# Optimization experiments

Hardware: AMD Instinct MI355X
Metric: run time of the kernel (lower is better)

## Reference

```python
import jax, jax.numpy as jnp
import numpy as np

D_MODEL = 512
NUM_HEADS = 8
VOCAB = 32000
B, TQ, TS = 4, 512, 512


def setup_inputs() -> dict:
    key = jax.random.key(0)
    ks = jax.random.split(key, 12)
    s = 1.0 / np.sqrt(D_MODEL)
    inp = {
        "src_vocab_size": VOCAB,
        "dec_output": jax.random.normal(ks[0], (B, TQ, D_MODEL), jnp.float32),
        "enc_output": jax.random.normal(ks[1], (B, TS, D_MODEL), jnp.float32),
        "src": jax.random.randint(ks[2], (B, TS), 0, VOCAB),
        "p1": jax.random.uniform(ks[3], (B, TQ, VOCAB), jnp.float32),
        # fcQ: d_model -> d_model (xavier)
        "WfcQ": jax.random.normal(ks[4], (D_MODEL, D_MODEL), jnp.float32) * s,
        "bfcQ": jnp.zeros((D_MODEL,), jnp.float32),
        # MHA query / key projections (V and output proj skipped in copy mode)
        "Wq": jax.random.normal(ks[5], (D_MODEL, D_MODEL), jnp.float32) * s,
        "bq": jnp.zeros((D_MODEL,), jnp.float32),
        "Wk": jax.random.normal(ks[6], (D_MODEL, D_MODEL), jnp.float32) * s,
        "bk": jnp.zeros((D_MODEL,), jnp.float32),
        # fcw: d_model -> 1 gate
        "Wfcw": jax.random.normal(ks[7], (1, D_MODEL), jnp.float32) * s,
        "bfcw": jnp.zeros((1,), jnp.float32),
    }
    return inp


def reference(src_vocab_size, dec_output, enc_output, src, p1,
              WfcQ, bfcQ, Wq, bq, Wk, bk, Wfcw, bfcw):
    b, tq, d = dec_output.shape
    h = NUM_HEADS
    dh = d // h
    # copy_query = fcQ(dec_output)
    cq = dec_output @ WfcQ.T + bfcQ
    # per-head Q, K projections
    Q = (cq @ Wq.T + bq).reshape(b, tq, h, dh).transpose(0, 2, 1, 3)          # [b,h,tq,dh]
    K = (enc_output @ Wk.T + bk).reshape(b, -1, h, dh).transpose(0, 2, 1, 3)  # [b,h,ts,dh]
    scale = 1.0 / jnp.sqrt(jnp.asarray(dh, dec_output.dtype))
    scores = jnp.einsum('bhqd,bhkd->bhqk', Q, K) * scale
    attn = jax.nn.softmax(scores, axis=-1).mean(axis=1)  # [b,tq,ts] head-averaged
    # attn @ one_hot(src, vocab)  ==  scatter-add of attn weights by src token id
    def scatter_copy(a, s):  # a: [tq,ts], s: [ts]
        return jax.ops.segment_sum(a.T, s, num_segments=src_vocab_size).T  # [tq,vocab]
    a_output = jax.vmap(scatter_copy)(attn, src)  # [b,tq,vocab]
    p2 = jax.nn.softmax(a_output, axis=-1)
    w = jax.nn.sigmoid(dec_output @ Wfcw.T + bfcw)  # [b,tq,1]
    return p2 * w + (1.0 - w) * p1
```

## Files before the change

kernel.cpp:

```cpp
#include <hip/hip_runtime.h>

constexpr int BATCH = 4;
constexpr int SEQ   = 512;
constexpr int DM    = 512;
constexpr int NH    = 8;
constexpr int NV    = 32000;
constexpr int NROWS = BATCH * SEQ;

typedef short short8 __attribute__((ext_vector_type(8)));
typedef float floatx4 __attribute__((ext_vector_type(4)));
typedef float floatv4 __attribute__((ext_vector_type(4)));

__device__ __forceinline__ float wave_reduce_max(float v) {
#pragma unroll
  for (int o = 32; o > 0; o >>= 1) v = fmaxf(v, __shfl_down(v, o, 64));
  return v;
}
__device__ __forceinline__ float wave_reduce_sum(float v) {
#pragma unroll
  for (int o = 32; o > 0; o >>= 1) v += __shfl_down(v, o, 64);
  return v;
}
__device__ __forceinline__ unsigned short f2bf(float f) {
  unsigned u = __float_as_uint(f);
  u += 0x7FFFu + ((u >> 16) & 1u);
  return (unsigned short)(u >> 16);
}
__device__ __forceinline__ float bf2f(unsigned short b) {
  return __uint_as_float(((unsigned)b) << 16);
}

__global__ __launch_bounds__(256)
void prep_kernel(const float* __restrict__ dec, const float* __restrict__ enc,
                 const float* __restrict__ Wk,
                 unsigned short* __restrict__ dec_bf, unsigned short* __restrict__ enc_bf,
                 unsigned short* __restrict__ wk_bf,
                 const int* __restrict__ src, int* __restrict__ map,
                 const float* __restrict__ Wq, const float* __restrict__ WfcQ,
                 unsigned short* __restrict__ wqc_bf,
                 const float* __restrict__ bfcQ, const float* __restrict__ bq,
                 float* __restrict__ bq2) {
  __shared__ float As[16][68];
  __shared__ float Bs[16][68];
  const int b = blockIdx.x, tid = threadIdx.x;
  if (b < 64) {
    const int m0 = (b >> 3) << 6, n0 = (b & 7) << 6;
    const int tx = tid & 15, ty = tid >> 4;
    const int r = tid >> 2, c = (tid & 3) << 2;
    float acc[4][4] = {};
    for (int k0 = 0; k0 < DM; k0 += 16) {
      const float4 av = *(const float4*)(Wq + (size_t)(m0 + r) * DM + k0 + c);
      As[c + 0][r] = av.x; As[c + 1][r] = av.y; As[c + 2][r] = av.z; As[c + 3][r] = av.w;
      const float4 bv = *(const float4*)(WfcQ + (size_t)(k0 + ty) * DM + n0 + (tx << 2));
      *(float4*)(&Bs[ty][tx << 2]) = bv;
      __syncthreads();
#pragma unroll
      for (int kk = 0; kk < 16; ++kk) {
        const float4 a4 = *(const float4*)(&As[kk][ty << 2]);
        const float4 b4 = *(const float4*)(&Bs[kk][tx << 2]);
        const float a[4] = {a4.x, a4.y, a4.z, a4.w};
        const float bb[4] = {b4.x, b4.y, b4.z, b4.w};
#pragma unroll
        for (int i = 0; i < 4; ++i)
#pragma unroll
          for (int j = 0; j < 4; ++j) acc[i][j] = fmaf(a[i], bb[j], acc[i][j]);
      }
      __syncthreads();
    }
#pragma unroll
    for (int i = 0; i < 4; ++i)
#pragma unroll
      for (int j = 0; j < 4; ++j)
        wqc_bf[(size_t)(m0 + (ty << 2) + i) * DM + n0 + (tx << 2) + j] = f2bf(acc[i][j]);
  } else if (b < 2368) {
    const int cb = b - 64;
    const float* in; unsigned short* outp; int i;
    if (cb < 1024)      { in = dec; outp = dec_bf; i = cb * 256 + tid; }
    else if (cb < 2048) { in = enc; outp = enc_bf; i = (cb - 1024) * 256 + tid; }
    else                { in = Wk;  outp = wk_bf;  i = (cb - 2048) * 256 + tid; }
    const float4 v = ((const float4*)in)[i];
    ushort4 o;
    o.x = f2bf(v.x); o.y = f2bf(v.y); o.z = f2bf(v.z); o.w = f2bf(v.w);
    ((ushort4*)outp)[i] = o;
  } else if (b < 2372) {
    const int bb = b - 2368;
    const int v0 = src[bb * SEQ + tid];
    atomicCAS(&map[(size_t)bb * NV + v0], -1, tid);
    const int v1 = src[bb * SEQ + tid + 256];
    atomicCAS(&map[(size_t)bb * NV + v1], -1, tid + 256);
  } else {
    const int h = tid >> 6, l = tid & 63;
    const int n = (b - 2372) * 4 + h;
    float s = 0.f;
#pragma unroll
    for (int t = 0; t < 8; ++t) {
      const int j = l + 64 * t;
      s = fmaf(Wq[(size_t)n * DM + j], bfcQ[j], s);
    }
    s = wave_reduce_sum(s);
    if (l == 0) bq2[n] = bq[n] + s;
  }
}

__global__ __launch_bounds__(256)
void gemm_mfma_kernel(const unsigned short* __restrict__ A0, const unsigned short* __restrict__ W0,
                      const float* __restrict__ b0, unsigned short* __restrict__ C0,
                      const unsigned short* __restrict__ A1, const unsigned short* __restrict__ W1,
                      const float* __restrict__ b1, unsigned short* __restrict__ C1) {
  const unsigned short* A; const unsigned short* W; const float* bias; unsigned short* C;
  if (blockIdx.z == 0) { A = A0; W = W0; bias = b0; C = C0; }
  else                 { A = A1; W = W1; bias = b1; C = C1; }
  const int m0 = blockIdx.y << 6, n0 = blockIdx.x << 6;
  __shared__ __align__(16) unsigned short As[64 * 72];
  __shared__ __align__(16) unsigned short Ws[64 * 72];
  const int tid = threadIdx.x;
  const int wv = tid >> 6, l = tid & 63;
  const int lm = l & 15, lq = l >> 4;
  floatx4 acc[4] = {};
  for (int k0 = 0; k0 < DM; k0 += 64) {
#pragma unroll
    for (int i = 0; i < 2; ++i) {
      const int ch = tid + (i << 8);
      const int row = ch >> 3, c8 = (ch & 7) << 3;
      *(int4*)(&As[row * 72 + c8]) = *(const int4*)(A + (size_t)(m0 + row) * DM + k0 + c8);
      *(int4*)(&Ws[row * 72 + c8]) = *(const int4*)(W + (size_t)(n0 + row) * DM + k0 + c8);
    }
    __syncthreads();
#pragma unroll
    for (int ks = 0; ks < 64; ks += 32) {
      const short8 a = *(const short8*)(&As[(16 * wv + lm) * 72 + ks + lq * 8]);
#pragma unroll
      for (int c = 0; c < 4; ++c) {
        const short8 b = *(const short8*)(&Ws[(16 * c + lm) * 72 + ks + lq * 8]);
        acc[c] = __builtin_amdgcn_mfma_f32_16x16x32_bf16(a, b, acc[c], 0, 0, 0);
      }
    }
    __syncthreads();
  }
#pragma unroll
  for (int c = 0; c < 4; ++c) {
    const float bv = bias[n0 + 16 * c + lm];
#pragma unroll
    for (int r = 0; r < 4; ++r)
      As[(16 * wv + lq * 4 + r) * 72 + 16 * c + lm] = f2bf(acc[c][r] + bv);
  }
  __syncthreads();
#pragma unroll
  for (int i = 0; i < 2; ++i) {
    const int idx = tid + (i << 8);
    const int row = idx >> 3, c8 = (idx & 7) << 3;
    *(int4*)(C + (size_t)(m0 + row) * DM + n0 + c8) = *(const int4*)(&As[row * 72 + c8]);
  }
}

__global__ __launch_bounds__(256)
void scores_mfma_kernel(const unsigned short* __restrict__ Q, const unsigned short* __restrict__ Kk,
                        unsigned short* __restrict__ scores) {
  const int bh = blockIdx.z, bb = bh >> 3, h = bh & 7;
  const int tq0 = blockIdx.y << 6, ts0 = blockIdx.x << 6;
  __shared__ __align__(16) unsigned short Qs[64 * 72];
  __shared__ __align__(16) unsigned short Ks[64 * 72];
  const int tid = threadIdx.x;
  const int wv = tid >> 6, l = tid & 63;
  const int lm = l & 15, lq = l >> 4;
#pragma unroll
  for (int i = 0; i < 2; ++i) {
    const int ch = tid + (i << 8);
    const int row = ch >> 3, c8 = (ch & 7) << 3;
    *(int4*)(&Qs[row * 72 + c8]) =
        *(const int4*)(Q + (size_t)(bb * SEQ + tq0 + row) * DM + h * 64 + c8);
    *(int4*)(&Ks[row * 72 + c8]) =
        *(const int4*)(Kk + (size_t)(bb * SEQ + ts0 + row) * DM + h * 64 + c8);
  }
  __syncthreads();
  floatx4 acc[4] = {};
#pragma unroll
  for (int ks = 0; ks < 64; ks += 32) {
    const short8 a = *(const short8*)(&Qs[(16 * wv + lm) * 72 + ks + lq * 8]);
#pragma unroll
    for (int c = 0; c < 4; ++c) {
      const short8 b = *(const short8*)(&Ks[(16 * c + lm) * 72 + ks + lq * 8]);
      acc[c] = __builtin_amdgcn_mfma_f32_16x16x32_bf16(a, b, acc[c], 0, 0, 0);
    }
  }
  __syncthreads();
#pragma unroll
  for (int c = 0; c < 4; ++c)
#pragma unroll
    for (int r = 0; r < 4; ++r)
      Qs[(16 * wv + lq * 4 + r) * 72 + 16 * c + lm] = f2bf(acc[c][r] * 0.125f);
  __syncthreads();
#pragma unroll
  for (int i = 0; i < 2; ++i) {
    const int idx = tid + (i << 8);
    const int row = idx >> 3, c8 = (idx & 7) << 3;
    *(int4*)(scores + ((size_t)bh * SEQ + tq0 + row) * SEQ + ts0 + c8) =
        *(const int4*)(&Qs[row * 72 + c8]);
  }
}

__global__ __launch_bounds__(512)
void softmax_fused_kernel(const unsigned short* __restrict__ scores, const int* __restrict__ src,
                          const int* __restrict__ map, const float* __restrict__ dec,
                          const float* __restrict__ Wfcw, const float* __restrict__ bfcw,
                          float* __restrict__ expa, float* __restrict__ row_a,
                          float* __restrict__ row_b) {
  __shared__ float hp[8 * 520];
  __shared__ float aslot[512];
  __shared__ float r1[8], r2[8];
  const int row = blockIdx.x, bb = row >> 9, tq = row & 511;
  const int tid = threadIdx.x, h = tid >> 6, l = tid & 63;
  aslot[tid] = 0.f;
  const unsigned short* srow = scores + ((size_t)(bb * NH + h) * SEQ + tq) * SEQ;
  union { int4 v; unsigned short u[8]; } U;
  U.v = *(const int4*)(srow + 8 * l);
  float s[8];
#pragma unroll
  for (int i = 0; i < 8; ++i) s[i] = bf2f(U.u[i]);
  float m = s[0];
#pragma unroll
  for (int i = 1; i < 8; ++i) m = fmaxf(m, s[i]);
  m = wave_reduce_max(m);
  m = __shfl(m, 0, 64);
  float e[8], sum = 0.f;
#pragma unroll
  for (int i = 0; i < 8; ++i) { e[i] = __expf(s[i] - m); sum += e[i]; }
  sum = wave_reduce_sum(sum);
  sum = __shfl(sum, 0, 64);
  const float inv = 1.f / sum;
  float4 p0, p1v;
  p0.x = e[0] * inv; p0.y = e[1] * inv; p0.z = e[2] * inv; p0.w = e[3] * inv;
  p1v.x = e[4] * inv; p1v.y = e[5] * inv; p1v.z = e[6] * inv; p1v.w = e[7] * inv;
  *(float4*)(&hp[h * 520 + 8 * l])     = p0;
  *(float4*)(&hp[h * 520 + 8 * l + 4]) = p1v;
  __syncthreads();
  float a = 0.f;
#pragma unroll
  for (int h2 = 0; h2 < 8; ++h2) a += hp[h2 * 520 + tid];
  a *= 0.125f;
  const int sv = src[bb * SEQ + tid];
  const int rep = map[(size_t)bb * NV + sv];
  atomicAdd(&aslot[rep], a);
  __syncthreads();
  const float ev = __expf(aslot[tid]);
  expa[(size_t)row * SEQ + tid] = ev;
  const float d = dec[(size_t)row * DM + tid] * Wfcw[tid];
  float es = wave_reduce_sum(ev);
  float ds = wave_reduce_sum(d);
  if (l == 0) { r1[h] = es; r2[h] = ds; }
  __syncthreads();
  if (tid == 0) {
    float esum = 0.f, dsum = bfcw[0];
#pragma unroll
    for (int i = 0; i < 8; ++i) { esum += r1[i]; dsum += r2[i]; }
    const float w = 1.f / (1.f + __expf(-dsum));
    row_a[row] = 1.f - w;
    row_b[row] = w / ((float)(NV - SEQ) + esum);
  }
}

__global__ __launch_bounds__(320)
void final_kernel(const float* __restrict__ p1, const int* __restrict__ map,
                  const float* __restrict__ expa, const float* __restrict__ row_a,
                  const float* __restrict__ row_b, float* __restrict__ out) {
  const int row = blockIdx.y;
  const int q4  = blockIdx.x * 320 + threadIdx.x;
  const int bb  = row >> 9;
  const size_t g = (size_t)row * (NV / 4) + q4;
  const floatv4 p = __builtin_nontemporal_load((const floatv4*)p1 + g);
  const int4 m = *(const int4*)(map + (size_t)bb * NV + (q4 << 2));
  const float ra = row_a[row], rb = row_b[row];
  const float* ea = expa + (size_t)row * SEQ;
  const float t0 = ea[m.x & 511];
  const float t1 = ea[m.y & 511];
  const float t2 = ea[m.z & 511];
  const float t3 = ea[m.w & 511];
  const float e0 = (m.x >= 0) ? t0 : 1.f;
  const float e1 = (m.y >= 0) ? t1 : 1.f;
  const float e2 = (m.z >= 0) ? t2 : 1.f;
  const float e3 = (m.w >= 0) ? t3 : 1.f;
  floatv4 o;
  o.x = fmaf(ra, p.x, rb * e0);
  o.y = fmaf(ra, p.y, rb * e1);
  o.z = fmaf(ra, p.z, rb * e2);
  o.w = fmaf(ra, p.w, rb * e3);
  __builtin_nontemporal_store(o, (floatv4*)out + g);
}

extern "C" void kernel_launch(void* const* d_in, const int* in_sizes, int n_in,
                              void* d_out, int out_size, void* d_ws, size_t ws_size,
                              hipStream_t stream) {
  const float* dec  = (const float*)d_in[1];
  const float* enc  = (const float*)d_in[2];
  const int*   src  = (const int*)d_in[3];
  const float* p1   = (const float*)d_in[4];
  const float* WfcQ = (const float*)d_in[5];
  const float* bfcQ = (const float*)d_in[6];
  const float* Wq   = (const float*)d_in[7];
  const float* bq   = (const float*)d_in[8];
  const float* Wk   = (const float*)d_in[9];
  const float* bk   = (const float*)d_in[10];
  const float* Wfcw = (const float*)d_in[11];
  const float* bfcw = (const float*)d_in[12];
  float* out = (float*)d_out;

  char* ws = (char*)d_ws;
  int*            map     = (int*)(ws);
  unsigned short* dec_bf  = (unsigned short*)(ws + (size_t)( 1 << 20));
  unsigned short* enc_bf  = (unsigned short*)(ws + (size_t)( 3 << 20));
  unsigned short* wk_bf   = (unsigned short*)(ws + (size_t)( 5 << 20));
  unsigned short* wqc_bf  = (unsigned short*)(ws + (size_t)( 5 << 20) + (512 << 10));
  float*          bq2     = (float*)(ws + (size_t)( 6 << 20));
  float*          row_a   = (float*)(ws + (size_t)( 6 << 20) + (64 << 10));
  float*          row_b   = (float*)(ws + (size_t)( 6 << 20) + (128 << 10));
  unsigned short* qlin_bf = (unsigned short*)(ws + (size_t)( 7 << 20));
  unsigned short* klin_bf = (unsigned short*)(ws + (size_t)( 9 << 20));
  float*          expa    = (float*)(ws + (size_t)(11 << 20));
  unsigned short* scores  = (unsigned short*)(ws + (size_t)(16 << 20));

  hipMemsetAsync(map, 0xFF, (size_t)BATCH * NV * sizeof(int), stream);

  prep_kernel<<<2500, 256, 0, stream>>>(dec, enc, Wk, dec_bf, enc_bf, wk_bf,
                                        src, map, Wq, WfcQ, wqc_bf, bfcQ, bq, bq2);

  gemm_mfma_kernel<<<dim3(8, 32, 2), 256, 0, stream>>>(
      dec_bf, wqc_bf, bq2, qlin_bf, enc_bf, wk_bf, bk, klin_bf);

  scores_mfma_kernel<<<dim3(8, 8, 32), 256, 0, stream>>>(qlin_bf, klin_bf, scores);

  softmax_fused_kernel<<<NROWS, 512, 0, stream>>>(scores, src, map, dec, Wfcw, bfcw,
                                                  expa, row_a, row_b);

  final_kernel<<<dim3(25, NROWS), 320, 0, stream>>>(p1, map, expa, row_a, row_b, out);
}
```

Measured before the change: 510.2 us.

## Fuse attention scores and softmax into one kernel, fold map init into prep

The separate scores MFMA kernel and the per-row softmax kernel are replaced by a single attn_kernel. In it, each wave computes one head's QK^T for 8 query rows over all 512 keys in registers, then does the softmax, head averaging via LDS atomics, the scatter by source token, the exp, and the gate reduction. This removes the bf16 scores buffer round trip through global memory and one kernel launch. The hipMemsetAsync of the map is replaced by in-kernel initialization inside the map-building blocks of prep_kernel. The cost is a large register footprint (32 accumulator tiles), half-wasted MFMA rows (16-row tiles for 8 query rows), LDS atomics, and only 256 blocks to cover the GPU.

```diff
diff --git a/kernel.cpp b/kernel.cpp
--- a/kernel.cpp
+++ b/kernel.cpp
@@ -84,6 +84,10 @@
     ((ushort4*)outp)[i] = o;
   } else if (b < 2372) {
     const int bb = b - 2368;
+    int4* mp = (int4*)(map + (size_t)bb * NV);
+    const int4 neg = make_int4(-1, -1, -1, -1);
+    for (int i = tid; i < NV / 4; i += 256) mp[i] = neg;
+    __syncthreads();
     const int v0 = src[bb * SEQ + tid];
     atomicCAS(&map[(size_t)bb * NV + v0], -1, tid);
     const int v1 = src[bb * SEQ + tid + 256];
@@ -153,109 +157,99 @@
   }
 }
 
-__global__ __launch_bounds__(256)
-void scores_mfma_kernel(const unsigned short* __restrict__ Q, const unsigned short* __restrict__ Kk,
-                        unsigned short* __restrict__ scores) {
-  const int bh = blockIdx.z, bb = bh >> 3, h = bh & 7;
-  const int tq0 = blockIdx.y << 6, ts0 = blockIdx.x << 6;
-  __shared__ __align__(16) unsigned short Qs[64 * 72];
-  __shared__ __align__(16) unsigned short Ks[64 * 72];
-  const int tid = threadIdx.x;
-  const int wv = tid >> 6, l = tid & 63;
+__global__ __launch_bounds__(512)
+void attn_kernel(const unsigned short* __restrict__ Q, const unsigned short* __restrict__ Kk,
+                 const int* __restrict__ src, const int* __restrict__ map,
+                 const float* __restrict__ dec, const float* __restrict__ Wfcw,
+                 const float* __restrict__ bfcw,
+                 float* __restrict__ expa, float* __restrict__ row_a,
+                 float* __restrict__ row_b) {
+  __shared__ float amean[8][520];
+  __shared__ float aslot[8][512];
+  const int bb = blockIdx.y, tq0 = blockIdx.x << 3;
+  const int tid = threadIdx.x, h = tid >> 6, l = tid & 63;
   const int lm = l & 15, lq = l >> 4;
-#pragma unroll
-  for (int i = 0; i < 2; ++i) {
-    const int ch = tid + (i << 8);
-    const int row = ch >> 3, c8 = (ch & 7) << 3;
-    *(int4*)(&Qs[row * 72 + c8]) =
-        *(const int4*)(Q + (size_t)(bb * SEQ + tq0 + row) * DM + h * 64 + c8);
-    *(int4*)(&Ks[row * 72 + c8]) =
-        *(const int4*)(Kk + (size_t)(bb * SEQ + ts0 + row) * DM + h * 64 + c8);
-  }
-  __syncthreads();
-  floatx4 acc[4] = {};
-#pragma unroll
-  for (int ks = 0; ks < 64; ks += 32) {
-    const short8 a = *(const short8*)(&Qs[(16 * wv + lm) * 72 + ks + lq * 8]);
-#pragma unroll
-    for (int c = 0; c < 4; ++c) {
-      const short8 b = *(const short8*)(&Ks[(16 * c + lm) * 72 + ks + lq * 8]);
-      acc[c] = __builtin_amdgcn_mfma_f32_16x16x32_bf16(a, b, acc[c], 0, 0, 0);
-    }
-  }
-  __syncthreads();
-#pragma unroll
-  for (int c = 0; c < 4; ++c)
-#pragma unroll
-    for (int r = 0; r < 4; ++r)
-      Qs[(16 * wv + lq * 4 + r) * 72 + 16 * c + lm] = f2bf(acc[c][r] * 0.125f);
-  __syncthreads();
-#pragma unroll
-  for (int i = 0; i < 2; ++i) {
-    const int idx = tid + (i << 8);
-    const int row = idx >> 3, c8 = (idx & 7) << 3;
-    *(int4*)(scores + ((size_t)bh * SEQ + tq0 + row) * SEQ + ts0 + c8) =
-        *(const int4*)(&Qs[row * 72 + c8]);
-  }
-}
-
-__global__ __launch_bounds__(512)
-void softmax_fused_kernel(const unsigned short* __restrict__ scores, const int* __restrict__ src,
-                          const int* __restrict__ map, const float* __restrict__ dec,
-                          const float* __restrict__ Wfcw, const float* __restrict__ bfcw,
-                          float* __restrict__ expa, float* __restrict__ row_a,
-                          float* __restrict__ row_b) {
-  __shared__ float hp[8 * 520];
-  __shared__ float aslot[512];
-  __shared__ float r1[8], r2[8];
-  const int row = blockIdx.x, bb = row >> 9, tq = row & 511;
-  const int tid = threadIdx.x, h = tid >> 6, l = tid & 63;
-  aslot[tid] = 0.f;
-  const unsigned short* srow = scores + ((size_t)(bb * NH + h) * SEQ + tq) * SEQ;
-  union { int4 v; unsigned short u[8]; } U;
-  U.v = *(const int4*)(srow + 8 * l);
-  float s[8];
-#pragma unroll
-  for (int i = 0; i < 8; ++i) s[i] = bf2f(U.u[i]);
-  float m = s[0];
-#pragma unroll
-  for (int i = 1; i < 8; ++i) m = fmaxf(m, s[i]);
-  m = wave_reduce_max(m);
-  m = __shfl(m, 0, 64);
-  float e[8], sum = 0.f;
-#pragma unroll
-  for (int i = 0; i < 8; ++i) { e[i] = __expf(s[i] - m); sum += e[i]; }
-  sum = wave_reduce_sum(sum);
-  sum = __shfl(sum, 0, 64);
-  const float inv = 1.f / sum;
-  float4 p0, p1v;
-  p0.x = e[0] * inv; p0.y = e[1] * inv; p0.z = e[2] * inv; p0.w = e[3] * inv;
-  p1v.x = e[4] * inv; p1v.y = e[5] * inv; p1v.z = e[6] * inv; p1v.w = e[7] * inv;
-  *(float4*)(&hp[h * 520 + 8 * l])     = p0;
-  *(float4*)(&hp[h * 520 + 8 * l + 4]) = p1v;
-  __syncthreads();
-  float a = 0.f;
-#pragma unroll
-  for (int h2 = 0; h2 < 8; ++h2) a += hp[h2 * 520 + tid];
-  a *= 0.125f;
+  for (int i = tid; i < 8 * 520; i += 512) ((float*)amean)[i] = 0.f;
+  for (int i = tid; i < 8 * 512; i += 512) ((float*)aslot)[i] = 0.f;
+  __syncthreads();
+
+  const size_t qrow = (size_t)(bb * SEQ + tq0 + lm) * DM + h * 64 + lq * 8;
+  const short8 qa0 = *(const short8*)(Q + qrow);
+  const short8 qa1 = *(const short8*)(Q + qrow + 32);
+  const unsigned short* kbase = Kk + (size_t)(bb * SEQ + lm) * DM + h * 64 + lq * 8;
+  floatx4 acc[32];
+#pragma unroll
+  for (int c = 0; c < 32; ++c) acc[c] = (floatx4){0.f, 0.f, 0.f, 0.f};
+#pragma unroll
+  for (int c = 0; c < 32; ++c) {
+    const short8 kb0 = *(const short8*)(kbase + (size_t)(16 * c) * DM);
+    const short8 kb1 = *(const short8*)(kbase + (size_t)(16 * c) * DM + 32);
+    acc[c] = __builtin_amdgcn_mfma_f32_16x16x32_bf16(qa0, kb0, acc[c], 0, 0, 0);
+    acc[c] = __builtin_amdgcn_mfma_f32_16x16x32_bf16(qa1, kb1, acc[c], 0, 0, 0);
+  }
+
+  float mx[4] = {-3.0e38f, -3.0e38f, -3.0e38f, -3.0e38f};
+#pragma unroll
+  for (int c = 0; c < 32; ++c)
+#pragma unroll
+    for (int r = 0; r < 4; ++r) mx[r] = fmaxf(mx[r], acc[c][r]);
+#pragma unroll
+  for (int r = 0; r < 4; ++r)
+#pragma unroll
+    for (int o = 8; o > 0; o >>= 1) mx[r] = fmaxf(mx[r], __shfl_xor(mx[r], o, 64));
+  float sm[4] = {0.f, 0.f, 0.f, 0.f};
+#pragma unroll
+  for (int c = 0; c < 32; ++c)
+#pragma unroll
+    for (int r = 0; r < 4; ++r) {
+      const float e = __expf(0.125f * (acc[c][r] - mx[r]));
+      acc[c][r] = e;
+      sm[r] += e;
+    }
+#pragma unroll
+  for (int r = 0; r < 4; ++r)
+#pragma unroll
+    for (int o = 8; o > 0; o >>= 1) sm[r] += __shfl_xor(sm[r], o, 64);
+  if (lq < 2) {
+#pragma unroll
+    for (int r = 0; r < 4; ++r) {
+      const float inv = 0.125f / sm[r];
+      const int row = lq * 4 + r;
+#pragma unroll
+      for (int c = 0; c < 32; ++c)
+        atomicAdd(&amean[row][16 * c + lm], acc[c][r] * inv);
+    }
+  }
+  __syncthreads();
+
   const int sv = src[bb * SEQ + tid];
   const int rep = map[(size_t)bb * NV + sv];
-  atomicAdd(&aslot[rep], a);
-  __syncthreads();
-  const float ev = __expf(aslot[tid]);
-  expa[(size_t)row * SEQ + tid] = ev;
-  const float d = dec[(size_t)row * DM + tid] * Wfcw[tid];
-  float es = wave_reduce_sum(ev);
-  float ds = wave_reduce_sum(d);
-  if (l == 0) { r1[h] = es; r2[h] = ds; }
-  __syncthreads();
-  if (tid == 0) {
-    float esum = 0.f, dsum = bfcw[0];
-#pragma unroll
-    for (int i = 0; i < 8; ++i) { esum += r1[i]; dsum += r2[i]; }
-    const float w = 1.f / (1.f + __expf(-dsum));
-    row_a[row] = 1.f - w;
-    row_b[row] = w / ((float)(NV - SEQ) + esum);
+#pragma unroll
+  for (int r = 0; r < 8; ++r) atomicAdd(&aslot[r][rep], amean[r][tid]);
+  __syncthreads();
+
+#pragma unroll
+  for (int r = 0; r < 8; ++r) {
+    const float ev = __expf(aslot[r][tid]);
+    expa[(size_t)(bb * SEQ + tq0 + r) * SEQ + tid] = ev;
+    amean[r][tid] = ev;
+  }
+  __syncthreads();
+
+  const int grow = bb * SEQ + tq0 + h;
+  float es = 0.f, ds = 0.f;
+#pragma unroll
+  for (int t = 0; t < 8; ++t) {
+    const int j = l + 64 * t;
+    es += amean[h][j];
+    ds = fmaf(dec[(size_t)grow * DM + j], Wfcw[j], ds);
+  }
+  es = wave_reduce_sum(es);
+  ds = wave_reduce_sum(ds);
+  if (l == 0) {
+    const float w = 1.f / (1.f + __expf(-(ds + bfcw[0])));
+    row_a[grow] = 1.f - w;
+    row_b[grow] = w / ((float)(NV - SEQ) + es);
   }
 }
 
@@ -316,9 +310,6 @@
   unsigned short* qlin_bf = (unsigned short*)(ws + (size_t)( 7 << 20));
   unsigned short* klin_bf = (unsigned short*)(ws + (size_t)( 9 << 20));
   float*          expa    = (float*)(ws + (size_t)(11 << 20));
-  unsigned short* scores  = (unsigned short*)(ws + (size_t)(16 << 20));
-
-  hipMemsetAsync(map, 0xFF, (size_t)BATCH * NV * sizeof(int), stream);
 
   prep_kernel<<<2500, 256, 0, stream>>>(dec, enc, Wk, dec_bf, enc_bf, wk_bf,
                                         src, map, Wq, WfcQ, wqc_bf, bfcQ, bq, bq2);
@@ -326,10 +317,8 @@
   gemm_mfma_kernel<<<dim3(8, 32, 2), 256, 0, stream>>>(
       dec_bf, wqc_bf, bq2, qlin_bf, enc_bf, wk_bf, bk, klin_bf);
 
-  scores_mfma_kernel<<<dim3(8, 8, 32), 256, 0, stream>>>(qlin_bf, klin_bf, scores);
-
-  softmax_fused_kernel<<<NROWS, 512, 0, stream>>>(scores, src, map, dec, Wfcw, bfcw,
-                                                  expa, row_a, row_b);
+  attn_kernel<<<dim3(64, BATCH), 512, 0, stream>>>(qlin_bf, klin_bf, src, map, dec,
+                                                   Wfcw, bfcw, expa, row_a, row_b);
 
   final_kernel<<<dim3(25, NROWS), 320, 0, stream>>>(p1, map, expa, row_a, row_b, out);
 }
```

Result: slower. 555.9 us (+9.0%).
